# Kernel optimization log

Hardware: AMD Instinct MI355X
Metric: run time of the kernel (lower is better)

Reference implementation:

```python
import jax, jax.numpy as jnp
import numpy as np

N_HEADS = 16

def setup_inputs() -> dict:
    key = jax.random.key(0)
    k0, k1, k2 = jax.random.split(key, 3)
    B, T, C = 4, 2048, 1024
    x = jax.random.normal(k0, (B, T, C), dtype=jnp.float32)
    # nn.Linear params: y = x @ W.T + b
    w_qkv = jax.random.normal(k1, (3 * C, C), dtype=jnp.float32) * 0.02
    b_qkv = jnp.zeros((3 * C,), dtype=jnp.float32)
    w_proj = jax.random.normal(k2, (C, C), dtype=jnp.float32) * 0.02
    b_proj = jnp.zeros((C,), dtype=jnp.float32)
    return {"x": x, "w_qkv": w_qkv, "b_qkv": b_qkv, "w_proj": w_proj, "b_proj": b_proj}

def reference(x, w_qkv, b_qkv, w_proj, b_proj):
    B, T, C = x.shape
    H = N_HEADS
    hd = C // H
    qkv = x @ w_qkv.T + b_qkv                      # [B, T, 3C]
    q, k, v = jnp.split(qkv, 3, axis=-1)           # each [B, T, C]
    q = q.reshape(B, T, H, hd).transpose(0, 2, 1, 3)  # [B, H, T, hd]
    k = k.reshape(B, T, H, hd).transpose(0, 2, 1, 3)
    v = v.reshape(B, T, H, hd).transpose(0, 2, 1, 3)
    # note: original scales by emb_dim**-0.5 (C), not head_dim**-0.5
    wei = jnp.einsum("bhqd,bhkd->bhqk", q, k) * (C ** -0.5)  # [B, H, T, T]
    causal = jnp.tril(jnp.ones((T, T), dtype=bool))
    wei = jnp.where(causal, wei, -jnp.inf)
    att = jax.nn.softmax(wei, axis=-1)
    out = jnp.einsum("bhqk,bhkd->bhqd", att, v)    # [B, H, T, hd]
    out = out.transpose(0, 2, 1, 3).reshape(B, T, C)
    return out @ w_proj.T + b_proj
```

## Files before the change

kernel.cpp:

```cpp
#include <hip/hip_runtime.h>
#include <hip/hip_bf16.h>

typedef __bf16 bf16;
typedef __bf16 bf16x8 __attribute__((ext_vector_type(8)));
typedef __bf16 bf16x4 __attribute__((ext_vector_type(4)));
typedef float  f32x4  __attribute__((ext_vector_type(4)));

#define LDS_ASYNC16(g, l)                                            \
  __builtin_amdgcn_global_load_lds(                                  \
      (const __attribute__((address_space(1))) void*)(g),            \
      (__attribute__((address_space(3))) void*)(l), 16, 0, 0)

#define QSCALE 0.04508421995f

__global__ void cvt3_f32_bf16(const float* __restrict__ i0, bf16* __restrict__ o0, int n0,
                              const float* __restrict__ i1, bf16* __restrict__ o1, int n1,
                              const float* __restrict__ i2, bf16* __restrict__ o2, int n2) {
  int i = blockIdx.x * blockDim.x + threadIdx.x;
  const float* in;
  bf16* out;
  if (i < n0) {
    in = i0; out = o0;
  } else if (i < n0 + n1) {
    i -= n0; in = i1; out = o1;
  } else {
    i -= n0 + n1;
    if (i >= n2) return;
    in = i2; out = o2;
  }
  float4 v = ((const float4*)in)[i];
  bf16x4 o = {(bf16)v.x, (bf16)v.y, (bf16)v.z, (bf16)v.w};
  ((bf16x4*)out)[i] = o;
}

template <int MODE>
__global__ __launch_bounds__(512, 2) void gemm_bt(
    const bf16* __restrict__ A, const bf16* __restrict__ B,
    const float* __restrict__ bias, float* __restrict__ outf,
    bf16* __restrict__ oq, bf16* __restrict__ ok, bf16* __restrict__ ov,
    int M, int N, int K) {
  __shared__ __align__(16) bf16 As[2][256 * 64];
  __shared__ __align__(16) bf16 Bs[2][128 * 64];
  const int tid = threadIdx.x;
  const int wave = tid >> 6, lane = tid & 63;
  const int quad = lane >> 4, l15 = lane & 15, l7 = l15 & 7;
  const int bm = blockIdx.x * 256, bn = blockIdx.y * 128;
  const int wrow = (wave >> 1) << 6;
  const int wcol = (wave & 1) << 6;

  f32x4 acc[4][4] = {};

  const int csw = ((tid & 7) ^ ((tid >> 3) & 7)) * 8;
  const bf16* gA = A + (size_t)(bm + (tid >> 3)) * K + csw;
  const bf16* gB = B + (size_t)(bn + (tid >> 3)) * K + csw;
  const size_t K64 = (size_t)K * 64;
  const int KT = K >> 6;

#define STAGE_TILE(kti, cb) do {                                      \
    const bf16* ak_ = gA + (size_t)(kti) * 64;                        \
    const bf16* bk_ = gB + (size_t)(kti) * 64;                        \
    char* la_ = (char*)As + (cb) * 32768 + wave * 1024;               \
    char* lb_ = (char*)Bs + (cb) * 16384 + wave * 1024;               \
    LDS_ASYNC16(ak_, la_);                                            \
    LDS_ASYNC16(ak_ + K64, la_ + 8192);                               \
    LDS_ASYNC16(ak_ + 2 * K64, la_ + 16384);                          \
    LDS_ASYNC16(ak_ + 3 * K64, la_ + 24576);                          \
    LDS_ASYNC16(bk_, lb_);                                            \
    LDS_ASYNC16(bk_ + K64, lb_ + 8192);                               \
  } while (0)

  STAGE_TILE(0, 0);
  STAGE_TILE(1, 1);

#pragma unroll 1
  for (int kt = 0; kt < KT; ++kt) {
    const int c = kt & 1;
    if (kt + 1 < KT)
      asm volatile("s_waitcnt vmcnt(6)" ::: "memory");
    else
      asm volatile("s_waitcnt vmcnt(0)" ::: "memory");
    __builtin_amdgcn_sched_barrier(0);
    __builtin_amdgcn_s_barrier();
    __builtin_amdgcn_sched_barrier(0);

    bf16x8 af[4][2], bfr[4][2];
    const char* baseA = (const char*)As + c * 32768;
    const char* baseB = (const char*)Bs + c * 16384;
#pragma unroll
    for (int mi = 0; mi < 4; ++mi) {
      const int row = wrow + mi * 16 + l15;
#pragma unroll
      for (int s = 0; s < 2; ++s)
        af[mi][s] = *(const bf16x8*)(baseA + row * 128 +
                                     (((s << 2) + quad) ^ l7) * 16);
    }
#pragma unroll
    for (int ni = 0; ni < 4; ++ni) {
      const int row = wcol + ni * 16 + l15;
#pragma unroll
      for (int s = 0; s < 2; ++s)
        bfr[ni][s] = *(const bf16x8*)(baseB + row * 128 +
                                      (((s << 2) + quad) ^ l7) * 16);
    }
    asm volatile("s_waitcnt lgkmcnt(0)" ::: "memory");
    __builtin_amdgcn_sched_barrier(0);
    __builtin_amdgcn_s_barrier();
    __builtin_amdgcn_sched_barrier(0);

    if (kt + 2 < KT) STAGE_TILE(kt + 2, c);

    __builtin_amdgcn_s_setprio(1);
#pragma unroll
    for (int s = 0; s < 2; ++s)
#pragma unroll
      for (int mi = 0; mi < 4; ++mi)
#pragma unroll
        for (int ni = 0; ni < 4; ++ni)
          acc[mi][ni] = __builtin_amdgcn_mfma_f32_16x16x32_bf16(
              af[mi][s], bfr[ni][s], acc[mi][ni], 0, 0, 0);
    __builtin_amdgcn_s_setprio(0);
  }
#undef STAGE_TILE

#pragma unroll
  for (int mi = 0; mi < 4; ++mi) {
    const int row0 = bm + wrow + mi * 16 + quad * 4;
#pragma unroll
    for (int ni = 0; ni < 4; ++ni) {
      const int col = bn + wcol + ni * 16 + l15;
      const float bv = bias[col];
      if (MODE == 0) {
#pragma unroll
        for (int r = 0; r < 4; ++r)
          outf[(size_t)(row0 + r) * N + col] = acc[mi][ni][r] + bv;
      } else {
        const int part = col >> 10;
        const int cn = col & 1023, h = cn >> 6, d = cn & 63;
        const int b = row0 >> 11, t0 = row0 & 2047;
        if (part == 2) {
          bf16x4 pk = {(bf16)(acc[mi][ni][0] + bv), (bf16)(acc[mi][ni][1] + bv),
                       (bf16)(acc[mi][ni][2] + bv), (bf16)(acc[mi][ni][3] + bv)};
          *(bf16x4*)(ov + ((size_t)(b * 16 + h) * 64 + d) * 2048 + t0) = pk;
        } else {
          const float sc = part ? 1.0f : QSCALE;
          bf16* dst = (part ? ok : oq) + ((size_t)(b * 16 + h) * 2048 + t0) * 64 + d;
#pragma unroll
          for (int r = 0; r < 4; ++r)
            dst[(size_t)r * 64] = (bf16)((acc[mi][ni][r] + bv) * sc);
        }
      }
    }
  }
}

__global__ __launch_bounds__(256) void flash_attn(
    const bf16* __restrict__ qb, const bf16* __restrict__ kb,
    const bf16* __restrict__ vt, bf16* __restrict__ ob) {
  constexpr int T = 2048;
  __shared__ bf16 Ks[2][64 * 72];
  __shared__ bf16 Vs[2][64 * 72];
  __shared__ float Ls[4][2][4][16];
  const int tid = threadIdx.x, wave = tid >> 6, lane = tid & 63;
  const int quad = lane >> 4, l15 = lane & 15;
  const int bh = blockIdx.x;
  const int b = bh >> 4, h = bh & 15;
  const bf16* qbase = qb + (size_t)bh * T * 64;
  const bf16* kbase = kb + (size_t)bh * T * 64;
  const bf16* vbase = vt + (size_t)bh * 64 * T;
  const int srow = tid >> 3, sc = (tid & 7) * 8;

  const int vp0 = (sc & ~31) | ((sc & 8) << 1) | ((sc & 16) >> 2);

  const int qt = 15 - (int)blockIdx.y;
  const int q0 = qt * 128 + wave * 32;

  bf16x8 qf[2][2];
#pragma unroll
  for (int qi = 0; qi < 2; ++qi)
#pragma unroll
    for (int ks = 0; ks < 2; ++ks)
      qf[qi][ks] = *(const bf16x8*)(qbase + (size_t)(q0 + qi * 16 + l15) * 64 +
                                    ks * 32 + quad * 8);

  f32x4 lsumv[2] = {};
  f32x4 oacc[2][4] = {};

  const int nkt = 2 * qt + 2;
  const int ktp = q0 >> 6;

  {
    uint4 k0 = *(const uint4*)(kbase + (size_t)srow * 64 + sc);
    uint4 k1 = *(const uint4*)(kbase + (size_t)(srow + 32) * 64 + sc);
    uint4 v0 = *(const uint4*)(vbase + (size_t)srow * T + sc);
    uint4 v1 = *(const uint4*)(vbase + (size_t)(srow + 32) * T + sc);
    *(uint4*)&Ks[0][srow * 72 + sc] = k0;
    *(uint4*)&Ks[0][(srow + 32) * 72 + sc] = k1;
    *(uint2*)&Vs[0][srow * 72 + vp0] = make_uint2(v0.x, v0.y);
    *(uint2*)&Vs[0][srow * 72 + vp0 + 8] = make_uint2(v0.z, v0.w);
    *(uint2*)&Vs[0][(srow + 32) * 72 + vp0] = make_uint2(v1.x, v1.y);
    *(uint2*)&Vs[0][(srow + 32) * 72 + vp0 + 8] = make_uint2(v1.z, v1.w);
  }

#pragma unroll 1
  for (int kt = 0; kt < nkt; ++kt) {
    __syncthreads();
    const int cur = kt & 1;
    const bool pre = (kt + 1) < nkt;
    uint4 pk0, pk1, pv0, pv1;
    if (pre) {
      const bf16* kp = kbase + (size_t)(kt + 1) * 64 * 64;
      const bf16* vp = vbase + (kt + 1) * 64;
      pk0 = *(const uint4*)(kp + (size_t)srow * 64 + sc);
      pk1 = *(const uint4*)(kp + (size_t)(srow + 32) * 64 + sc);
      pv0 = *(const uint4*)(vp + (size_t)srow * T + sc);
      pv1 = *(const uint4*)(vp + (size_t)(srow + 32) * T + sc);
    }
    if (kt <= ktp) {
      f32x4 st[4][2];
      __builtin_amdgcn_s_setprio(1);
#pragma unroll
      for (int ki = 0; ki < 4; ++ki) {
        bf16x8 kfa = *(const bf16x8*)&Ks[cur][(ki * 16 + l15) * 72 + quad * 8];
        bf16x8 kfb =
            *(const bf16x8*)&Ks[cur][(ki * 16 + l15) * 72 + 32 + quad * 8];
#pragma unroll
        for (int qi = 0; qi < 2; ++qi) {
          f32x4 a = {0.f, 0.f, 0.f, 0.f};
          a = __builtin_amdgcn_mfma_f32_16x16x32_bf16(kfa, qf[qi][0], a, 0, 0, 0);
          a = __builtin_amdgcn_mfma_f32_16x16x32_bf16(kfb, qf[qi][1], a, 0, 0, 0);
          st[ki][qi] = a;
        }
      }
      __builtin_amdgcn_s_setprio(0);
      if (kt == ktp) {
#pragma unroll
        for (int ki = 0; ki < 4; ++ki)
#pragma unroll
          for (int qi = 0; qi < 2; ++qi)
#pragma unroll
            for (int r = 0; r < 4; ++r) {
              const int kcol = kt * 64 + ki * 16 + quad * 4 + r;
              const int qrow = q0 + qi * 16 + l15;
              if (kcol > qrow) st[ki][qi][r] = -__builtin_inff();
            }
      }
#pragma unroll
      for (int ki = 0; ki < 4; ++ki)
#pragma unroll
        for (int qi = 0; qi < 2; ++qi) {
#pragma unroll
          for (int r = 0; r < 4; ++r)
            st[ki][qi][r] = __builtin_amdgcn_exp2f(st[ki][qi][r]);
          lsumv[qi] += st[ki][qi];
        }
      bf16x8 pa8[2][2];
#pragma unroll
      for (int ki2 = 0; ki2 < 2; ++ki2)
#pragma unroll
        for (int qi = 0; qi < 2; ++qi) {
          bf16x8 p;
#pragma unroll
          for (int r = 0; r < 4; ++r) {
            p[r] = (bf16)st[2 * ki2][qi][r];
            p[r + 4] = (bf16)st[2 * ki2 + 1][qi][r];
          }
          pa8[ki2][qi] = p;
        }
      __builtin_amdgcn_s_setprio(1);
#pragma unroll
      for (int di = 0; di < 4; ++di)
#pragma unroll
        for (int ki2 = 0; ki2 < 2; ++ki2) {
          bf16x8 vv = *(const bf16x8*)&Vs[cur][(di * 16 + l15) * 72 + ki2 * 32 +
                                              quad * 8];
#pragma unroll
          for (int qi = 0; qi < 2; ++qi)
            oacc[qi][di] = __builtin_amdgcn_mfma_f32_16x16x32_bf16(
                pa8[ki2][qi], vv, oacc[qi][di], 0, 0, 0);
        }
      __builtin_amdgcn_s_setprio(0);
    }
    if (pre) {
      const int nxt = cur ^ 1;
      *(uint4*)&Ks[nxt][srow * 72 + sc] = pk0;
      *(uint4*)&Ks[nxt][(srow + 32) * 72 + sc] = pk1;
      *(uint2*)&Vs[nxt][srow * 72 + vp0] = make_uint2(pv0.x, pv0.y);
      *(uint2*)&Vs[nxt][srow * 72 + vp0 + 8] = make_uint2(pv0.z, pv0.w);
      *(uint2*)&Vs[nxt][(srow + 32) * 72 + vp0] = make_uint2(pv1.x, pv1.y);
      *(uint2*)&Vs[nxt][(srow + 32) * 72 + vp0 + 8] = make_uint2(pv1.z, pv1.w);
    }
  }

#pragma unroll
  for (int qi = 0; qi < 2; ++qi)
    Ls[wave][qi][quad][l15] =
        lsumv[qi][0] + lsumv[qi][1] + lsumv[qi][2] + lsumv[qi][3];
#pragma unroll
  for (int qi = 0; qi < 2; ++qi)
#pragma unroll
    for (int r = 0; r < 4; ++r) {
      const int rloc = quad * 4 + r;
      const float l = Ls[wave][qi][0][rloc] + Ls[wave][qi][1][rloc] +
                      Ls[wave][qi][2][rloc] + Ls[wave][qi][3][rloc];
      const float inv = 1.f / l;
      const int t = q0 + qi * 16 + rloc;
#pragma unroll
      for (int di = 0; di < 4; ++di) {
        const int d = di * 16 + l15;
        ob[((size_t)b * 2048 + t) * 1024 + h * 64 + d] =
            (bf16)(oacc[qi][di][r] * inv);
      }
    }
}

extern "C" void kernel_launch(void* const* d_in, const int* in_sizes, int n_in,
                              void* d_out, int out_size, void* d_ws,
                              size_t ws_size, hipStream_t stream) {
  const float* x = (const float*)d_in[0];
  const float* w_qkv = (const float*)d_in[1];
  const float* b_qkv = (const float*)d_in[2];
  const float* w_proj = (const float*)d_in[3];
  const float* b_proj = (const float*)d_in[4];
  float* out = (float*)d_out;

  const int B = 4, T = 2048, C = 1024;
  const size_t nx = (size_t)B * T * C;

  char* ws = (char*)d_ws;
  bf16* xb = (bf16*)ws;      ws += nx * 2;
  bf16* wqkvb = (bf16*)ws;   ws += (size_t)3 * C * C * 2;
  bf16* wprojb = (bf16*)ws;  ws += (size_t)C * C * 2;
  bf16* qb = (bf16*)ws;      ws += nx * 2;
  bf16* kbuf = (bf16*)ws;    ws += nx * 2;
  bf16* vtb = (bf16*)ws;     ws += nx * 2;
  bf16* attb = (bf16*)ws;    ws += nx * 2;

  const int n0 = (int)(nx / 4), n1 = 3 * C * C / 4, n2 = C * C / 4;
  cvt3_f32_bf16<<<(n0 + n1 + n2 + 255) / 256, 256, 0, stream>>>(
      x, xb, n0, w_qkv, wqkvb, n1, w_proj, wprojb, n2);

  dim3 g1(32, 24);
  gemm_bt<1><<<g1, 512, 0, stream>>>(xb, wqkvb, b_qkv, nullptr, qb, kbuf, vtb,
                                     B * T, 3 * C, C);
  dim3 g2(64, 16);
  flash_attn<<<g2, 256, 0, stream>>>(qb, kbuf, vtb, attb);

  dim3 g3(32, 8);
  gemm_bt<0><<<g3, 512, 0, stream>>>(attb, wprojb, b_proj, out, nullptr,
                                     nullptr, nullptr, B * T, C, C);
}
```

Before: 238.2 us.

## Enlarge GEMM tile to 256x256 with phased load/MFMA interleaving

Doubles the N dimension of each GEMM block tile to 256 and splits every K-step into four MFMA phases. The LDS fills for later stages are interleaved with these phases to overlap global loads with compute. The aim is to raise arithmetic intensity and LDS reuse per block. The cost is occupancy of one block per CU and fewer blocks in total, which leaves many CUs idle for the smaller projection GEMM.

```diff
diff --git a/kernel.cpp b/kernel.cpp
--- a/kernel.cpp
+++ b/kernel.cpp
@@ -34,100 +34,164 @@
 }
 
 template <int MODE>
-__global__ __launch_bounds__(512, 2) void gemm_bt(
+__global__ __launch_bounds__(512, 1) void gemm_bt(
     const bf16* __restrict__ A, const bf16* __restrict__ B,
     const float* __restrict__ bias, float* __restrict__ outf,
     bf16* __restrict__ oq, bf16* __restrict__ ok, bf16* __restrict__ ov,
     int M, int N, int K) {
   __shared__ __align__(16) bf16 As[2][256 * 64];
-  __shared__ __align__(16) bf16 Bs[2][128 * 64];
+  __shared__ __align__(16) bf16 Bs[2][256 * 64];
   const int tid = threadIdx.x;
   const int wave = tid >> 6, lane = tid & 63;
   const int quad = lane >> 4, l15 = lane & 15, l7 = l15 & 7;
-  const int bm = blockIdx.x * 256, bn = blockIdx.y * 128;
-  const int wrow = (wave >> 1) << 6;
-  const int wcol = (wave & 1) << 6;
-
-  f32x4 acc[4][4] = {};
+  const int wm = wave >> 2, wn = wave & 3;
+  const int bm = blockIdx.x * 256, bn = blockIdx.y * 256;
+
+  f32x4 acc[8][4] = {};
 
   const int csw = ((tid & 7) ^ ((tid >> 3) & 7)) * 8;
   const bf16* gA = A + (size_t)(bm + (tid >> 3)) * K + csw;
   const bf16* gB = B + (size_t)(bn + (tid >> 3)) * K + csw;
-  const size_t K64 = (size_t)K * 64;
   const int KT = K >> 6;
 
-#define STAGE_TILE(kti, cb) do {                                      \
-    const bf16* ak_ = gA + (size_t)(kti) * 64;                        \
-    const bf16* bk_ = gB + (size_t)(kti) * 64;                        \
-    char* la_ = (char*)As + (cb) * 32768 + wave * 1024;               \
-    char* lb_ = (char*)Bs + (cb) * 16384 + wave * 1024;               \
-    LDS_ASYNC16(ak_, la_);                                            \
-    LDS_ASYNC16(ak_ + K64, la_ + 8192);                               \
-    LDS_ASYNC16(ak_ + 2 * K64, la_ + 16384);                          \
-    LDS_ASYNC16(ak_ + 3 * K64, la_ + 24576);                          \
-    LDS_ASYNC16(bk_, lb_);                                            \
-    LDS_ASYNC16(bk_ + K64, lb_ + 8192);                               \
-  } while (0)
-
-  STAGE_TILE(0, 0);
-  STAGE_TILE(1, 1);
+#define ST_A(kt, cb, rb)                                               \
+  LDS_ASYNC16(gA + (size_t)(rb) * K + (size_t)(kt) * 64,               \
+              (char*)As + (cb) * 32768 + (rb) * 128 + wave * 1024)
+#define ST_B(kt, cb, rb)                                               \
+  LDS_ASYNC16(gB + (size_t)(rb) * K + (size_t)(kt) * 64,               \
+              (char*)Bs + (cb) * 32768 + (rb) * 128 + wave * 1024)
+
+  ST_A(0, 0, 0);   ST_A(0, 0, 128);
+  ST_B(0, 0, 0);   ST_B(0, 0, 64);
+  ST_A(0, 0, 64);  ST_A(0, 0, 192);
+  ST_B(0, 0, 128); ST_B(0, 0, 192);
+  ST_A(1, 1, 0);   ST_A(1, 1, 128);
+  ST_B(1, 1, 0);   ST_B(1, 1, 64);
+  ST_A(1, 1, 64);  ST_A(1, 1, 192);
+  asm volatile("s_waitcnt vmcnt(6)" ::: "memory");
+  __builtin_amdgcn_sched_barrier(0);
+  __builtin_amdgcn_s_barrier();
+  __builtin_amdgcn_sched_barrier(0);
+
+  const int rowA = wm * 128 + l15;
+  const int rowB = wn * 64 + l15;
+  const int c0 = (quad ^ l7) * 16, c1 = ((4 + quad) ^ l7) * 16;
 
 #pragma unroll 1
   for (int kt = 0; kt < KT; ++kt) {
     const int c = kt & 1;
-    if (kt + 1 < KT)
-      asm volatile("s_waitcnt vmcnt(6)" ::: "memory");
-    else
-      asm volatile("s_waitcnt vmcnt(0)" ::: "memory");
-    __builtin_amdgcn_sched_barrier(0);
-    __builtin_amdgcn_s_barrier();
-    __builtin_amdgcn_sched_barrier(0);
-
-    bf16x8 af[4][2], bfr[4][2];
-    const char* baseA = (const char*)As + c * 32768;
-    const char* baseB = (const char*)Bs + c * 16384;
+    const char* bA = (const char*)As + c * 32768;
+    const char* bB = (const char*)Bs + c * 32768;
+    bf16x8 af[4][2], bg0[2][2], bg1[2][2];
+
 #pragma unroll
     for (int mi = 0; mi < 4; ++mi) {
-      const int row = wrow + mi * 16 + l15;
-#pragma unroll
-      for (int s = 0; s < 2; ++s)
-        af[mi][s] = *(const bf16x8*)(baseA + row * 128 +
-                                     (((s << 2) + quad) ^ l7) * 16);
-    }
+      af[mi][0] = *(const bf16x8*)(bA + (rowA + mi * 16) * 128 + c0);
+      af[mi][1] = *(const bf16x8*)(bA + (rowA + mi * 16) * 128 + c1);
+    }
+#pragma unroll
+    for (int ni = 0; ni < 2; ++ni) {
+      bg0[ni][0] = *(const bf16x8*)(bB + (rowB + ni * 16) * 128 + c0);
+      bg0[ni][1] = *(const bf16x8*)(bB + (rowB + ni * 16) * 128 + c1);
+    }
+    if (kt + 1 < KT) { ST_B(kt + 1, c ^ 1, 128); ST_B(kt + 1, c ^ 1, 192); }
+    __builtin_amdgcn_sched_barrier(0);
+    __builtin_amdgcn_s_barrier();
+    asm volatile("s_waitcnt lgkmcnt(0)" ::: "memory");
+    __builtin_amdgcn_sched_barrier(0);
+    __builtin_amdgcn_s_setprio(1);
+#pragma unroll
+    for (int s = 0; s < 2; ++s)
+#pragma unroll
+      for (int mi = 0; mi < 4; ++mi)
+#pragma unroll
+        for (int ni = 0; ni < 2; ++ni)
+          acc[mi][ni] = __builtin_amdgcn_mfma_f32_16x16x32_bf16(
+              af[mi][s], bg0[ni][s], acc[mi][ni], 0, 0, 0);
+    __builtin_amdgcn_s_setprio(0);
+    __builtin_amdgcn_sched_barrier(0);
+    __builtin_amdgcn_s_barrier();
+
+#pragma unroll
+    for (int ni = 0; ni < 2; ++ni) {
+      bg1[ni][0] = *(const bf16x8*)(bB + (rowB + 32 + ni * 16) * 128 + c0);
+      bg1[ni][1] = *(const bf16x8*)(bB + (rowB + 32 + ni * 16) * 128 + c1);
+    }
+    if (kt + 2 < KT) { ST_A(kt + 2, c, 0); ST_A(kt + 2, c, 128); }
+    __builtin_amdgcn_sched_barrier(0);
+    __builtin_amdgcn_s_barrier();
+    asm volatile("s_waitcnt lgkmcnt(0)" ::: "memory");
+    __builtin_amdgcn_sched_barrier(0);
+    __builtin_amdgcn_s_setprio(1);
+#pragma unroll
+    for (int s = 0; s < 2; ++s)
+#pragma unroll
+      for (int mi = 0; mi < 4; ++mi)
+#pragma unroll
+        for (int ni = 0; ni < 2; ++ni)
+          acc[mi][ni + 2] = __builtin_amdgcn_mfma_f32_16x16x32_bf16(
+              af[mi][s], bg1[ni][s], acc[mi][ni + 2], 0, 0, 0);
+    __builtin_amdgcn_s_setprio(0);
+    __builtin_amdgcn_sched_barrier(0);
+    __builtin_amdgcn_s_barrier();
+
+#pragma unroll
+    for (int mi = 0; mi < 4; ++mi) {
+      af[mi][0] = *(const bf16x8*)(bA + (rowA + 64 + mi * 16) * 128 + c0);
+      af[mi][1] = *(const bf16x8*)(bA + (rowA + 64 + mi * 16) * 128 + c1);
+    }
+    if (kt + 2 < KT) { ST_B(kt + 2, c, 0); ST_B(kt + 2, c, 64); }
+    __builtin_amdgcn_sched_barrier(0);
+    __builtin_amdgcn_s_barrier();
+    asm volatile("s_waitcnt lgkmcnt(0)" ::: "memory");
+    __builtin_amdgcn_sched_barrier(0);
+    __builtin_amdgcn_s_setprio(1);
+#pragma unroll
+    for (int s = 0; s < 2; ++s)
+#pragma unroll
+      for (int mi = 0; mi < 4; ++mi)
+#pragma unroll
+        for (int ni = 0; ni < 2; ++ni)
+          acc[mi + 4][ni + 2] = __builtin_amdgcn_mfma_f32_16x16x32_bf16(
+              af[mi][s], bg1[ni][s], acc[mi + 4][ni + 2], 0, 0, 0);
+    __builtin_amdgcn_s_setprio(0);
+    __builtin_amdgcn_sched_barrier(0);
+    __builtin_amdgcn_s_barrier();
+
+    if (kt + 2 < KT) { ST_A(kt + 2, c, 64); ST_A(kt + 2, c, 192); }
+    __builtin_amdgcn_sched_barrier(0);
+    __builtin_amdgcn_s_barrier();
+    __builtin_amdgcn_sched_barrier(0);
+    __builtin_amdgcn_s_setprio(1);
+#pragma unroll
+    for (int s = 0; s < 2; ++s)
+#pragma unroll
+      for (int mi = 0; mi < 4; ++mi)
+#pragma unroll
+        for (int ni = 0; ni < 2; ++ni)
+          acc[mi + 4][ni] = __builtin_amdgcn_mfma_f32_16x16x32_bf16(
+              af[mi][s], bg0[ni][s], acc[mi + 4][ni], 0, 0, 0);
+    __builtin_amdgcn_s_setprio(0);
+    __builtin_amdgcn_sched_barrier(0);
+    if (kt + 1 < KT) {
+      if (kt + 2 < KT)
+        asm volatile("s_waitcnt vmcnt(6)" ::: "memory");
+      else
+        asm volatile("s_waitcnt vmcnt(0)" ::: "memory");
+      __builtin_amdgcn_sched_barrier(0);
+      __builtin_amdgcn_s_barrier();
+      __builtin_amdgcn_sched_barrier(0);
+    }
+  }
+#undef ST_A
+#undef ST_B
+
+#pragma unroll
+  for (int mi = 0; mi < 8; ++mi) {
+    const int row0 = bm + wm * 128 + mi * 16 + quad * 4;
 #pragma unroll
     for (int ni = 0; ni < 4; ++ni) {
-      const int row = wcol + ni * 16 + l15;
-#pragma unroll
-      for (int s = 0; s < 2; ++s)
-        bfr[ni][s] = *(const bf16x8*)(baseB + row * 128 +
-                                      (((s << 2) + quad) ^ l7) * 16);
-    }
-    asm volatile("s_waitcnt lgkmcnt(0)" ::: "memory");
-    __builtin_amdgcn_sched_barrier(0);
-    __builtin_amdgcn_s_barrier();
-    __builtin_amdgcn_sched_barrier(0);
-
-    if (kt + 2 < KT) STAGE_TILE(kt + 2, c);
-
-    __builtin_amdgcn_s_setprio(1);
-#pragma unroll
-    for (int s = 0; s < 2; ++s)
-#pragma unroll
-      for (int mi = 0; mi < 4; ++mi)
-#pragma unroll
-        for (int ni = 0; ni < 4; ++ni)
-          acc[mi][ni] = __builtin_amdgcn_mfma_f32_16x16x32_bf16(
-              af[mi][s], bfr[ni][s], acc[mi][ni], 0, 0, 0);
-    __builtin_amdgcn_s_setprio(0);
-  }
-#undef STAGE_TILE
-
-#pragma unroll
-  for (int mi = 0; mi < 4; ++mi) {
-    const int row0 = bm + wrow + mi * 16 + quad * 4;
-#pragma unroll
-    for (int ni = 0; ni < 4; ++ni) {
-      const int col = bn + wcol + ni * 16 + l15;
+      const int col = bn + wn * 64 + ni * 16 + l15;
       const float bv = bias[col];
       if (MODE == 0) {
 #pragma unroll
@@ -339,13 +403,13 @@
   cvt3_f32_bf16<<<(n0 + n1 + n2 + 255) / 256, 256, 0, stream>>>(
       x, xb, n0, w_qkv, wqkvb, n1, w_proj, wprojb, n2);
 
-  dim3 g1(32, 24);
+  dim3 g1(32, 12);
   gemm_bt<1><<<g1, 512, 0, stream>>>(xb, wqkvb, b_qkv, nullptr, qb, kbuf, vtb,
                                      B * T, 3 * C, C);
   dim3 g2(64, 16);
   flash_attn<<<g2, 256, 0, stream>>>(qb, kbuf, vtb, attb);
 
-  dim3 g3(32, 8);
+  dim3 g3(32, 4);
   gemm_bt<0><<<g3, 512, 0, stream>>>(attb, wprojb, b_proj, out, nullptr,
                                      nullptr, nullptr, B * T, C, C);
 }
```

New measurement: 259.8 us. 9.1% more time.
